# Kernel tuning notes

Hardware: AMD Instinct MI355X
Metric: run time of the kernel (lower is better)

Reference implementation:

```python
import jax, jax.numpy as jnp
import numpy as np

B, T, E, H, G = 8, 1024, 1024, 16, 4
D = E // H
SCALING = D ** -0.5
READER_W = 0.1  # reader_group_weight


def _heads(x):
    # [B, T, E] -> [B, H, T, D]
    return x.reshape(B, T, H, D).transpose(0, 2, 1, 3)


def setup_inputs() -> dict:
    key = jax.random.key(0)
    ks = jax.random.split(key, 16)
    s = 0.02
    return {
        "hidden_states": jax.random.normal(ks[0], (B, T, E), jnp.float32),
        "reader_token": jax.random.randint(ks[1], (B,), 0, G, dtype=jnp.int32),
        # shared (generic) projections, torch Linear convention: y = x @ W.T + b
        "Wq": jax.random.normal(ks[2], (E, E), jnp.float32) * s,
        "bq": jnp.zeros((E,), jnp.float32),
        "Wk": jax.random.normal(ks[3], (E, E), jnp.float32) * s,
        "bk": jnp.zeros((E,), jnp.float32),
        "Wv": jax.random.normal(ks[4], (E, E), jnp.float32) * s,
        "bv": jnp.zeros((E,), jnp.float32),
        "Wo": jax.random.normal(ks[5], (E, E), jnp.float32) * s,
        "bo": jnp.zeros((E,), jnp.float32),
        # stacked per-reader-group expert projections [G, E, E]
        "RWq": jax.random.normal(ks[6], (G, E, E), jnp.float32) * s,
        "Rbq": jnp.zeros((G, E), jnp.float32),
        "RWk": jax.random.normal(ks[7], (G, E, E), jnp.float32) * s,
        "Rbk": jnp.zeros((G, E), jnp.float32),
        "RWv": jax.random.normal(ks[8], (G, E, E), jnp.float32) * s,
        "Rbv": jnp.zeros((G, E), jnp.float32),
    }


def reference(hidden_states, reader_token, Wq, bq, Wk, bk, Wv, bv, Wo, bo,
              RWq, Rbq, RWk, Rbk, RWv, Rbv):
    hs = hidden_states
    # --- generic attention probs (shared weights) ---
    q = _heads((hs @ Wq.T + bq) * SCALING)          # [B,H,T,D]
    k = _heads(hs @ Wk.T + bk)                       # [B,H,T,D]
    v = _heads(hs @ Wv.T + bv)                       # [B,H,T,D]
    gen_probs = jax.nn.softmax(jnp.einsum('bhtd,bhsd->bhts', q, k), axis=-1)
    # --- reader-group attention probs (per-sample routed weights) ---
    Wq_b = RWq[reader_token]                          # [B,E,E]
    Wk_b = RWk[reader_token]
    q_r = _heads((jnp.einsum('bte,boe->bto', hs, Wq_b) + Rbq[reader_token][:, None, :]) * SCALING)
    k_r = _heads(jnp.einsum('bte,boe->bto', hs, Wk_b) + Rbk[reader_token][:, None, :])
    rdr_probs = jax.nn.softmax(jnp.einsum('bhtd,bhsd->bhts', q_r, k_r), axis=-1)
    # --- weighted combine, then attend over GENERIC value states ---
    probs = (READER_W * rdr_probs + (1.0 - READER_W) * gen_probs) / 2.0
    attn = jnp.einsum('bhts,bhsd->bhtd', probs, v)    # [B,H,T,D]
    attn = attn.transpose(0, 2, 1, 3).reshape(B, T, E)
    return attn @ Wo.T + bo
```

## Files before the change

kernel.cpp:

```cpp
#include <hip/hip_runtime.h>
#include <stdint.h>

#define AS1 __attribute__((address_space(1)))
#define AS3 __attribute__((address_space(3)))

typedef __attribute__((ext_vector_type(8))) short bf16x8;
typedef __attribute__((ext_vector_type(4))) float f32x4;

#define NB 8
#define NT 1024
#define NE 1024
#define NH 16
#define BT (NB * NT)

__device__ __forceinline__ unsigned short f2bf(float f) {
    unsigned int u = __builtin_bit_cast(unsigned int, f);
    u += 0x7FFFu + ((u >> 16) & 1u);
    return (unsigned short)(u >> 16);
}
__device__ __forceinline__ unsigned int cvt_pk_bf16(float lo, float hi) {
    unsigned int r;
    asm("v_cvt_pk_bf16_f32 %0, %1, %2" : "=v"(r) : "v"(lo), "v"(hi));
    return r;
}

__global__ void k_cvt7(const float* __restrict__ hs, unsigned short* __restrict__ hsB,
                       const float* __restrict__ w1, unsigned short* __restrict__ w1B,
                       const float* __restrict__ w2, unsigned short* __restrict__ w2B,
                       const float* __restrict__ w3, unsigned short* __restrict__ w3B,
                       const float* __restrict__ w4, unsigned short* __restrict__ w4B,
                       const float* __restrict__ r1, unsigned short* __restrict__ r1B,
                       const float* __restrict__ r2, unsigned short* __restrict__ r2B)
{
    int blk = blockIdx.x;
    const float* s; unsigned short* d; int base;
    if      (blk < 8192)  { s = hs; d = hsB; base = 0; }
    else if (blk < 9216)  { s = w1; d = w1B; base = 8192; }
    else if (blk < 10240) { s = w2; d = w2B; base = 9216; }
    else if (blk < 11264) { s = w3; d = w3B; base = 10240; }
    else if (blk < 12288) { s = w4; d = w4B; base = 11264; }
    else if (blk < 16384) { s = r1; d = r1B; base = 12288; }
    else                  { s = r2; d = r2B; base = 16384; }
    int i = ((blk - base) * 256 + threadIdx.x) * 4;
    float4 f = *reinterpret_cast<const float4*>(s + i);
    ushort4 o;
    o.x = f2bf(f.x); o.y = f2bf(f.y); o.z = f2bf(f.z); o.w = f2bf(f.w);
    *reinterpret_cast<ushort4*>(d + i) = o;
}

struct GJob {
    const unsigned short* W;
    const float* bias;
    void* out;
    float scale;
    int routed;
};

template <bool OUT_F32>
__global__ __launch_bounds__(512, 2)
void k_gemm256(const unsigned short* __restrict__ A,
               GJob j0, GJob j1, GJob j2, GJob j3, GJob j4,
               const int* __restrict__ rt)
{
    __shared__ __attribute__((aligned(16))) unsigned short LB[2][2][2][128 * 64];

    const int flat = blockIdx.x;
    const int xcd = flat & 7;
    const int l   = flat >> 3;
    const int pz  = l >> 4;
    const int r   = l & 15;
    const int by  = xcd * 4 + (r >> 2);
    const int bx  = r & 3;
    const int m0 = by << 8, n0 = bx << 8;

    GJob jb = j0;
    if (pz == 1) jb = j1;
    else if (pz == 2) jb = j2;
    else if (pz == 3) jb = j3;
    else if (pz == 4) jb = j4;
    int g = jb.routed ? rt[m0 >> 10] : 0;
    const unsigned short* Wg = jb.W + (size_t)g * NE * NE;

    const int tid  = threadIdx.x;
    const int wid  = tid >> 6;
    const int lane = tid & 63;
    const int frow = lane & 15;
    const int g4   = lane >> 4;
    const int wm = wid >> 2, wn = wid & 3;

    const int rh0  = tid >> 3;
    const int swz8 = ((tid & 7) ^ (rh0 & 7)) * 8;
    const unsigned short* baseA = A  + (size_t)m0 * NE;
    const unsigned short* baseB = Wg + (size_t)n0 * NE;

    auto STAGE = [&](int d, int mat, int half, int kt) {
        const unsigned short* base = mat ? baseB : baseA;
#pragma unroll
        for (int j = 0; j < 2; ++j) {
            const unsigned short* src =
                base + (size_t)(half * 128 + rh0 + j * 64) * NE + kt * 64 + swz8;
            __builtin_amdgcn_global_load_lds((AS1 void*)src,
                (AS3 void*)&LB[d][mat][half][(wid * 64 + j * 512) * 8], 16, 0, 0);
        }
    };

    f32x4 acc[8][4];
#pragma unroll
    for (int m = 0; m < 8; ++m)
#pragma unroll
        for (int n = 0; n < 4; ++n) acc[m][n] = (f32x4){0.f, 0.f, 0.f, 0.f};

    bf16x8 a4[4], b4[4];
    auto RDA = [&](int d, int mh, int kh) {
#pragma unroll
        for (int mf = 0; mf < 4; ++mf) {
            int rh = mh * 64 + mf * 16 + frow;
            int off = rh * 64 + (((kh * 4 + g4) ^ (frow & 7)) * 8);
            a4[mf] = *reinterpret_cast<const bf16x8*>(&LB[d][0][wm][off]);
        }
    };
    auto RDB = [&](int d, int kh) {
#pragma unroll
        for (int nf = 0; nf < 4; ++nf) {
            int rh = (wn & 1) * 64 + nf * 16 + frow;
            int off = rh * 64 + (((kh * 4 + g4) ^ (frow & 7)) * 8);
            b4[nf] = *reinterpret_cast<const bf16x8*>(&LB[d][1][wn >> 1][off]);
        }
    };
    auto MM = [&](int mh) {
        __builtin_amdgcn_s_setprio(1);
#pragma unroll
        for (int mf = 0; mf < 4; ++mf)
#pragma unroll
            for (int nf = 0; nf < 4; ++nf)
                acc[mh * 4 + mf][nf] =
                    __builtin_amdgcn_mfma_f32_16x16x32_bf16(a4[mf], b4[nf], acc[mh * 4 + mf][nf], 0, 0, 0);
        __builtin_amdgcn_s_setprio(0);
    };

#define BARX __builtin_amdgcn_s_barrier()
#define LGK0 asm volatile("s_waitcnt lgkmcnt(0)" ::: "memory")
#define VMC2 asm volatile("s_waitcnt vmcnt(2)" ::: "memory")
#define VMC0 asm volatile("s_waitcnt vmcnt(0)" ::: "memory")

    STAGE(0, 0, 0, 0); STAGE(0, 0, 1, 0); STAGE(0, 1, 0, 0); STAGE(0, 1, 1, 0);
    STAGE(1, 1, 0, 1);
    VMC2; BARX;

#pragma unroll 1
    for (int i = 0; i < 8; ++i) {
        const int t = 2 * i;
        const bool pre = (i < 7);
        RDA(0, 0, 0); RDB(0, 0); STAGE(1, 1, 1, t + 1); STAGE(1, 0, 1, t + 1);
        BARX; LGK0; MM(0); BARX;
        RDA(0, 1, 0); STAGE(1, 0, 0, t + 1);
        BARX; LGK0; MM(1); BARX;
        RDA(0, 0, 1); RDB(0, 1);
        BARX; LGK0; MM(0); BARX;
        RDA(0, 1, 1); if (pre) STAGE(0, 1, 0, t + 2);
        BARX; LGK0; MM(1); if (pre) { VMC2; } else { VMC0; } BARX;
        RDA(1, 0, 0); RDB(1, 0); if (pre) { STAGE(0, 1, 1, t + 2); STAGE(0, 0, 1, t + 2); }
        BARX; LGK0; MM(0); BARX;
        RDA(1, 1, 0); if (pre) STAGE(0, 0, 0, t + 2);
        BARX; LGK0; MM(1); BARX;
        RDA(1, 0, 1); RDB(1, 1);
        BARX; LGK0; MM(0); BARX;
        RDA(1, 1, 1); if (pre) STAGE(1, 1, 0, t + 3);
        BARX; LGK0; MM(1); VMC2; BARX;
    }
#undef BARX
#undef LGK0
#undef VMC2
#undef VMC0

    const float* biasg = jb.bias + (size_t)(jb.routed ? (rt[m0 >> 10]) : 0) * NE;
#pragma unroll
    for (int am = 0; am < 8; ++am) {
        int row = m0 + wm * 128 + am * 16 + g4 * 4;
#pragma unroll
        for (int nf = 0; nf < 4; ++nf) {
            int col = n0 + wn * 64 + nf * 16 + frow;
            float bv = biasg[col];
            f32x4 v = acc[am][nf];
#pragma unroll
            for (int r2 = 0; r2 < 4; ++r2) {
                float val = (v[r2] + bv) * jb.scale;
                if (OUT_F32)
                    ((float*)jb.out)[(size_t)(row + r2) * NE + col] = val;
                else
                    ((unsigned short*)jb.out)[(size_t)(row + r2) * NE + col] = f2bf(val);
            }
        }
    }
}

__global__ void k_vtrans(const unsigned short* __restrict__ V, unsigned short* __restrict__ Vt) {
    __shared__ unsigned short tile[64][65];
    const int blk = blockIdx.x;
    const int bh = blk >> 4;
    const int b = bh >> 4;
    const int h = bh & 15;
    const int s0 = (blk & 15) * 64;
    const int tid = threadIdx.x;
#pragma unroll
    for (int i = 0; i < 2; ++i) {
        int seg = tid + i * 256;
        int row = seg >> 3;
        int c8 = (seg & 7) * 8;
        const unsigned short* src = V + (size_t)(b * NT + s0 + row) * NE + h * 64 + c8;
        ushort4 u0 = *reinterpret_cast<const ushort4*>(src);
        ushort4 u1 = *reinterpret_cast<const ushort4*>(src + 4);
        tile[row][c8 + 0] = u0.x; tile[row][c8 + 1] = u0.y;
        tile[row][c8 + 2] = u0.z; tile[row][c8 + 3] = u0.w;
        tile[row][c8 + 4] = u1.x; tile[row][c8 + 5] = u1.y;
        tile[row][c8 + 6] = u1.z; tile[row][c8 + 7] = u1.w;
    }
    __syncthreads();
#pragma unroll
    for (int i = 0; i < 2; ++i) {
        int seg = tid + i * 256;
        int drow = seg >> 3;
        int s8 = (seg & 7) * 8;
        ushort4 u0, u1;
        u0.x = tile[s8 + 0][drow]; u0.y = tile[s8 + 1][drow];
        u0.z = tile[s8 + 2][drow]; u0.w = tile[s8 + 3][drow];
        u1.x = tile[s8 + 4][drow]; u1.y = tile[s8 + 5][drow];
        u1.z = tile[s8 + 6][drow]; u1.w = tile[s8 + 7][drow];
        unsigned short* dst = Vt + (size_t)(bh * 64 + drow) * NT + s0 + s8;
        *reinterpret_cast<ushort4*>(dst) = u0;
        *reinterpret_cast<ushort4*>(dst + 4) = u1;
    }
}

__global__ __launch_bounds__(512, 4)
void k_attn(const unsigned short* __restrict__ Q,
            const unsigned short* __restrict__ K,
            const unsigned short* __restrict__ Qr,
            const unsigned short* __restrict__ Kr,
            const unsigned short* __restrict__ Vt,
            unsigned short* __restrict__ attnO)
{
    constexpr int PLD = 40;
    __shared__ __attribute__((aligned(16))) unsigned short KV[2][3 * 4096];
    __shared__ __attribute__((aligned(16))) unsigned short Pga[8][16 * PLD];
    __shared__ __attribute__((aligned(16))) unsigned short Pra[8][16 * PLD];

    const int blk = (blockIdx.x & 7) * 128 + (blockIdx.x >> 3);
    const int tile = blk & 7;
    const int bh = blk >> 3;
    const int b = bh >> 4;
    const int h = bh & 15;
    const int wid = threadIdx.x >> 6;
    const int lane = threadIdx.x & 63;
    const int frow = lane & 15;
    const int g4 = lane >> 4;
    const int f7 = frow & 7;
    const int fk8 = g4 * 8;
    const int t0 = tile * 128 + wid * 16;

    const size_t qoff = (size_t)(b * NT + t0 + frow) * NE + h * 64;
    const bf16x8 qf0 = *reinterpret_cast<const bf16x8*>(Q + qoff + fk8);
    const bf16x8 qf1 = *reinterpret_cast<const bf16x8*>(Q + qoff + 32 + fk8);
    const bf16x8 qr0 = *reinterpret_cast<const bf16x8*>(Qr + qoff + fk8);
    const bf16x8 qr1 = *reinterpret_cast<const bf16x8*>(Qr + qoff + 32 + fk8);

    const unsigned short* Kb  = K  + (size_t)b * NT * NE + h * 64;
    const unsigned short* Krb = Kr + (size_t)b * NT * NE + h * 64;
    const unsigned short* Vtb = Vt + (size_t)bh * 64 * NT;
    unsigned short* PgRow = &Pga[wid][0] + frow * PLD;
    unsigned short* PrRow = &Pra[wid][0] + frow * PLD;

    f32x4 og[4], orr[4];
    float lgp = 0.f, lrp = 0.f;
#pragma unroll
    for (int i = 0; i < 4; ++i) {
        og[i] = (f32x4){0.f, 0.f, 0.f, 0.f};
        orr[i] = (f32x4){0.f, 0.f, 0.f, 0.f};
    }

    const int srow = threadIdx.x >> 3;
    const int scb8 = ((threadIdx.x & 7) ^ (srow & 7)) * 8;
    auto stage = [&](int buf, int s0) {
        const unsigned short* sK = Kb  + (size_t)(s0 + srow) * NE + scb8;
        const unsigned short* sR = Krb + (size_t)(s0 + srow) * NE + scb8;
        const unsigned short* sV = Vtb + (size_t)srow * NT + s0 + scb8;
        __builtin_amdgcn_global_load_lds((AS1 void*)sK, (AS3 void*)(&KV[buf][wid * 512]), 16, 0, 0);
        __builtin_amdgcn_global_load_lds((AS1 void*)sR, (AS3 void*)(&KV[buf][4096 + wid * 512]), 16, 0, 0);
        __builtin_amdgcn_global_load_lds((AS1 void*)sV, (AS3 void*)(&KV[buf][8192 + wid * 512]), 16, 0, 0);
    };

    stage(0, 0);
    __syncthreads();
    int cur = 0;
    const f32x4 z = (f32x4){0.f, 0.f, 0.f, 0.f};
#pragma unroll 1
    for (int t = 0; t < NT / 64; ++t) {
        if (t < NT / 64 - 1) stage(cur ^ 1, (t + 1) * 64);
        const unsigned short* Kl  = &KV[cur][0];
        const unsigned short* Krl = &KV[cur][4096];
        const unsigned short* Vl  = &KV[cur][8192];

        f32x4 sg[4], sr[4];
#pragma unroll
        for (int nf = 0; nf < 4; ++nf) {
            const int ro = (nf * 16 + frow) * 64;
            bf16x8 kA = *reinterpret_cast<const bf16x8*>(Kl + ro + ((g4 ^ f7) * 8));
            bf16x8 kB = *reinterpret_cast<const bf16x8*>(Kl + ro + (((4 + g4) ^ f7) * 8));
            bf16x8 rA = *reinterpret_cast<const bf16x8*>(Krl + ro + ((g4 ^ f7) * 8));
            bf16x8 rB = *reinterpret_cast<const bf16x8*>(Krl + ro + (((4 + g4) ^ f7) * 8));
            sg[nf] = __builtin_amdgcn_mfma_f32_16x16x32_bf16(kA, qf0, z, 0, 0, 0);
            sg[nf] = __builtin_amdgcn_mfma_f32_16x16x32_bf16(kB, qf1, sg[nf], 0, 0, 0);
            sr[nf] = __builtin_amdgcn_mfma_f32_16x16x32_bf16(rA, qr0, z, 0, 0, 0);
            sr[nf] = __builtin_amdgcn_mfma_f32_16x16x32_bf16(rB, qr1, sr[nf], 0, 0, 0);
        }

#pragma unroll
        for (int hh = 0; hh < 2; ++hh) {
#pragma unroll
            for (int j = 0; j < 2; ++j) {
                const int nf = 2 * hh + j;
                float g0 = __expf(sg[nf][0]), g1 = __expf(sg[nf][1]);
                float g2 = __expf(sg[nf][2]), g3 = __expf(sg[nf][3]);
                lgp += (g0 + g1) + (g2 + g3);
                uint2 wg;
                wg.x = cvt_pk_bf16(g0, g1);
                wg.y = cvt_pk_bf16(g2, g3);
                *reinterpret_cast<uint2*>(PgRow + j * 16 + g4 * 4) = wg;
                float r0 = __expf(sr[nf][0]), r1 = __expf(sr[nf][1]);
                float r2 = __expf(sr[nf][2]), r3 = __expf(sr[nf][3]);
                lrp += (r0 + r1) + (r2 + r3);
                uint2 wr;
                wr.x = cvt_pk_bf16(r0, r1);
                wr.y = cvt_pk_bf16(r2, r3);
                *reinterpret_cast<uint2*>(PrRow + j * 16 + g4 * 4) = wr;
            }
            asm volatile("s_waitcnt lgkmcnt(0)" ::: "memory");
            bf16x8 pg = *reinterpret_cast<const bf16x8*>(PgRow + fk8);
            bf16x8 pr = *reinterpret_cast<const bf16x8*>(PrRow + fk8);
            __builtin_amdgcn_s_setprio(1);
#pragma unroll
            for (int nf2 = 0; nf2 < 4; ++nf2) {
                const int vo = (nf2 * 16 + frow) * 64;
                bf16x8 v = *reinterpret_cast<const bf16x8*>(Vl + vo + (((4 * hh + g4) ^ f7) * 8));
                og[nf2]  = __builtin_amdgcn_mfma_f32_16x16x32_bf16(pg, v, og[nf2], 0, 0, 0);
                orr[nf2] = __builtin_amdgcn_mfma_f32_16x16x32_bf16(pr, v, orr[nf2], 0, 0, 0);
            }
            __builtin_amdgcn_s_setprio(0);
        }

        __syncthreads();
        cur ^= 1;
    }

    lgp += __shfl_xor(lgp, 16); lgp += __shfl_xor(lgp, 32);
    lrp += __shfl_xor(lrp, 16); lrp += __shfl_xor(lrp, 32);
    float ig = 0.45f / lgp, ir = 0.05f / lrp;
    float igr[4], irr[4];
#pragma unroll
    for (int r = 0; r < 4; ++r) {
        igr[r] = __shfl(ig, g4 * 4 + r);
        irr[r] = __shfl(ir, g4 * 4 + r);
    }
#pragma unroll
    for (int nf2 = 0; nf2 < 4; ++nf2) {
#pragma unroll
        for (int r = 0; r < 4; ++r) {
            float val = og[nf2][r] * igr[r] + orr[nf2][r] * irr[r];
            int tq = t0 + g4 * 4 + r;
            attnO[(size_t)(b * NT + tq) * NE + h * 64 + nf2 * 16 + frow] = f2bf(val);
        }
    }
}

extern "C" void kernel_launch(void* const* d_in, const int* in_sizes, int n_in,
                              void* d_out, int out_size, void* d_ws, size_t ws_size,
                              hipStream_t stream)
{
    const float* hs  = (const float*)d_in[0];
    const int*   rt  = (const int*)d_in[1];
    const float* Wq  = (const float*)d_in[2];
    const float* bq  = (const float*)d_in[3];
    const float* Wk  = (const float*)d_in[4];
    const float* bk  = (const float*)d_in[5];
    const float* Wv  = (const float*)d_in[6];
    const float* bv  = (const float*)d_in[7];
    const float* Wo  = (const float*)d_in[8];
    const float* bo  = (const float*)d_in[9];
    const float* RWq = (const float*)d_in[10];
    const float* Rbq = (const float*)d_in[11];
    const float* RWk = (const float*)d_in[12];
    const float* Rbk = (const float*)d_in[13];

    unsigned short* w = (unsigned short*)d_ws;
    const size_t NBT = (size_t)BT * NE;
    const size_t NW  = (size_t)NE * NE;
    unsigned short* hsB  = w; w += NBT;
    unsigned short* Qb   = w; w += NBT;
    unsigned short* Kb   = w; w += NBT;
    unsigned short* Vb   = w; w += NBT;
    unsigned short* Qrb  = w; w += NBT;
    unsigned short* Krb  = w; w += NBT;
    unsigned short* Vtb  = w; w += NBT;
    unsigned short* atb  = w; w += NBT;
    unsigned short* WqB  = w; w += NW;
    unsigned short* WkB  = w; w += NW;
    unsigned short* WvB  = w; w += NW;
    unsigned short* WoB  = w; w += NW;
    unsigned short* RWqB = w; w += 4 * NW;
    unsigned short* RWkB = w; w += 4 * NW;

    k_cvt7<<<dim3(20480), dim3(256), 0, stream>>>(hs, hsB, Wq, WqB, Wk, WkB, Wv, WvB,
                                                  Wo, WoB, RWq, RWqB, RWk, RWkB);

    GJob jq  = { WqB,  bq,  Qb,  0.125f, 0 };
    GJob jk  = { WkB,  bk,  Kb,  1.0f,   0 };
    GJob jv  = { WvB,  bv,  Vb,  1.0f,   0 };
    GJob jrq = { RWqB, Rbq, Qrb, 0.125f, 1 };
    GJob jrk = { RWkB, Rbk, Krb, 1.0f,   1 };
    k_gemm256<false><<<dim3(640), dim3(512), 0, stream>>>(hsB, jq, jk, jv, jrq, jrk, rt);

    k_vtrans<<<dim3(NB * NH * 16), dim3(256), 0, stream>>>(Vb, Vtb);
    k_attn<<<dim3(NB * NH * 8), dim3(512), 0, stream>>>(Qb, Kb, Qrb, Krb, Vtb, atb);

    GJob jo = { WoB, bo, d_out, 1.0f, 0 };
    k_gemm256<true><<<dim3(128), dim3(512), 0, stream>>>(atb, jo, jo, jo, jo, jo, nullptr);
}
```

Baseline: 241.1 us.

## Rework projection GEMM into 256x128 tiles with triple-buffered K=32 pipeline

Replaces the 256x256-tile, 8-wave GEMM with a 256x128-tile, 4-wave kernel. It uses a three-stage LDS ring of K=32 slices with a new XOR swizzle, and prefetches two slices ahead under vmcnt(6) waits. Grid sizes double, which gives more blocks for better CU fill, especially on the 128-block output projection. In exchange, each block reuses less data from a smaller tile and the K loop has more barriers per unit of work.

After: 243.9 us. No clear change (+1.2%).

```diff
diff --git a/kernel.cpp b/kernel.cpp
--- a/kernel.cpp
+++ b/kernel.cpp
@@ -57,21 +57,22 @@
 };
 
 template <bool OUT_F32>
-__global__ __launch_bounds__(512, 2)
-void k_gemm256(const unsigned short* __restrict__ A,
-               GJob j0, GJob j1, GJob j2, GJob j3, GJob j4,
-               const int* __restrict__ rt)
+__global__ __launch_bounds__(256, 2)
+void k_gemmP(const unsigned short* __restrict__ A,
+             GJob j0, GJob j1, GJob j2, GJob j3, GJob j4,
+             const int* __restrict__ rt)
 {
-    __shared__ __attribute__((aligned(16))) unsigned short LB[2][2][2][128 * 64];
+    __shared__ __attribute__((aligned(16))) unsigned short LA[3][256 * 32];
+    __shared__ __attribute__((aligned(16))) unsigned short LBb[3][128 * 32];
 
     const int flat = blockIdx.x;
     const int xcd = flat & 7;
     const int l   = flat >> 3;
-    const int pz  = l >> 4;
-    const int r   = l & 15;
-    const int by  = xcd * 4 + (r >> 2);
-    const int bx  = r & 3;
-    const int m0 = by << 8, n0 = bx << 8;
+    const int pz  = l >> 5;
+    const int r   = l & 31;
+    const int by  = xcd * 4 + (r >> 3);
+    const int bx  = r & 7;
+    const int m0 = by << 8, n0 = bx << 7;
 
     GJob jb = j0;
     if (pz == 1) jb = j1;
@@ -86,21 +87,31 @@
     const int lane = tid & 63;
     const int frow = lane & 15;
     const int g4   = lane >> 4;
-    const int wm = wid >> 2, wn = wid & 3;
-
-    const int rh0  = tid >> 3;
-    const int swz8 = ((tid & 7) ^ (rh0 & 7)) * 8;
+    const int wm = wid >> 1, wn = wid & 1;
+
     const unsigned short* baseA = A  + (size_t)m0 * NE;
     const unsigned short* baseB = Wg + (size_t)n0 * NE;
 
-    auto STAGE = [&](int d, int mat, int half, int kt) {
-        const unsigned short* base = mat ? baseB : baseA;
+    auto STAGE_A = [&](int buf, int kt) {
+#pragma unroll
+        for (int j = 0; j < 4; ++j) {
+            int c = tid + j * 256;
+            int row = c >> 2, cb = c & 3;
+            const unsigned short* src = baseA + (size_t)row * NE + kt * 32
+                                        + ((cb ^ ((row >> 1) & 3)) * 8);
+            __builtin_amdgcn_global_load_lds((AS1 void*)src,
+                (AS3 void*)(&LA[buf][0] + c * 8), 16, 0, 0);
+        }
+    };
+    auto STAGE_B = [&](int buf, int kt) {
 #pragma unroll
         for (int j = 0; j < 2; ++j) {
-            const unsigned short* src =
-                base + (size_t)(half * 128 + rh0 + j * 64) * NE + kt * 64 + swz8;
+            int c = tid + j * 256;
+            int row = c >> 2, cb = c & 3;
+            const unsigned short* src = baseB + (size_t)row * NE + kt * 32
+                                        + ((cb ^ ((row >> 1) & 3)) * 8);
             __builtin_amdgcn_global_load_lds((AS1 void*)src,
-                (AS3 void*)&LB[d][mat][half][(wid * 64 + j * 512) * 8], 16, 0, 0);
+                (AS3 void*)(&LBb[buf][0] + c * 8), 16, 0, 0);
         }
     };
 
@@ -111,20 +122,20 @@
         for (int n = 0; n < 4; ++n) acc[m][n] = (f32x4){0.f, 0.f, 0.f, 0.f};
 
     bf16x8 a4[4], b4[4];
-    auto RDA = [&](int d, int mh, int kh) {
+    auto RDA = [&](int buf, int mh) {
 #pragma unroll
         for (int mf = 0; mf < 4; ++mf) {
-            int rh = mh * 64 + mf * 16 + frow;
-            int off = rh * 64 + (((kh * 4 + g4) ^ (frow & 7)) * 8);
-            a4[mf] = *reinterpret_cast<const bf16x8*>(&LB[d][0][wm][off]);
-        }
-    };
-    auto RDB = [&](int d, int kh) {
+            int row = wm * 128 + mh * 64 + mf * 16 + frow;
+            a4[mf] = *reinterpret_cast<const bf16x8*>(
+                &LA[buf][row * 32 + ((g4 ^ ((row >> 1) & 3)) * 8)]);
+        }
+    };
+    auto RDB = [&](int buf) {
 #pragma unroll
         for (int nf = 0; nf < 4; ++nf) {
-            int rh = (wn & 1) * 64 + nf * 16 + frow;
-            int off = rh * 64 + (((kh * 4 + g4) ^ (frow & 7)) * 8);
-            b4[nf] = *reinterpret_cast<const bf16x8*>(&LB[d][1][wn >> 1][off]);
+            int row = wn * 64 + nf * 16 + frow;
+            b4[nf] = *reinterpret_cast<const bf16x8*>(
+                &LBb[buf][row * 32 + ((g4 ^ ((row >> 1) & 3)) * 8)]);
         }
     };
     auto MM = [&](int mh) {
@@ -140,40 +151,33 @@
 
 #define BARX __builtin_amdgcn_s_barrier()
 #define LGK0 asm volatile("s_waitcnt lgkmcnt(0)" ::: "memory")
-#define VMC2 asm volatile("s_waitcnt vmcnt(2)" ::: "memory")
+#define VMC6 asm volatile("s_waitcnt vmcnt(6)" ::: "memory")
 #define VMC0 asm volatile("s_waitcnt vmcnt(0)" ::: "memory")
 
-    STAGE(0, 0, 0, 0); STAGE(0, 0, 1, 0); STAGE(0, 1, 0, 0); STAGE(0, 1, 1, 0);
-    STAGE(1, 1, 0, 1);
-    VMC2; BARX;
-
+    STAGE_A(0, 0); STAGE_B(0, 0); STAGE_A(1, 1); STAGE_B(1, 1);
+    VMC6; BARX;
+
+    int bt = 0;
 #pragma unroll 1
-    for (int i = 0; i < 8; ++i) {
-        const int t = 2 * i;
-        const bool pre = (i < 7);
-        RDA(0, 0, 0); RDB(0, 0); STAGE(1, 1, 1, t + 1); STAGE(1, 0, 1, t + 1);
+    for (int t = 0; t < 32; ++t) {
+        const int b2 = (bt + 2 >= 3) ? bt - 1 : bt + 2;
+        const bool pre = (t + 2 < 32);
+        RDA(bt, 0); RDB(bt);
+        if (pre) STAGE_A(b2, t + 2);
         BARX; LGK0; MM(0); BARX;
-        RDA(0, 1, 0); STAGE(1, 0, 0, t + 1);
-        BARX; LGK0; MM(1); BARX;
-        RDA(0, 0, 1); RDB(0, 1);
-        BARX; LGK0; MM(0); BARX;
-        RDA(0, 1, 1); if (pre) STAGE(0, 1, 0, t + 2);
-        BARX; LGK0; MM(1); if (pre) { VMC2; } else { VMC0; } BARX;
-        RDA(1, 0, 0); RDB(1, 0); if (pre) { STAGE(0, 1, 1, t + 2); STAGE(0, 0, 1, t + 2); }
-        BARX; LGK0; MM(0); BARX;
-        RDA(1, 1, 0); if (pre) STAGE(0, 0, 0, t + 2);
-        BARX; LGK0; MM(1); BARX;
-        RDA(1, 0, 1); RDB(1, 1);
-        BARX; LGK0; MM(0); BARX;
-        RDA(1, 1, 1); if (pre) STAGE(1, 1, 0, t + 3);
-        BARX; LGK0; MM(1); VMC2; BARX;
+        RDA(bt, 1);
+        if (pre) STAGE_B(b2, t + 2);
+        BARX; LGK0; MM(1);
+        if (t < 30) { VMC6; } else if (t == 30) { VMC0; }
+        BARX;
+        bt = (bt + 1 >= 3) ? 0 : bt + 1;
     }
 #undef BARX
 #undef LGK0
-#undef VMC2
+#undef VMC6
 #undef VMC0
 
-    const float* biasg = jb.bias + (size_t)(jb.routed ? (rt[m0 >> 10]) : 0) * NE;
+    const float* biasg = jb.bias + (size_t)g * NE;
 #pragma unroll
     for (int am = 0; am < 8; ++am) {
         int row = m0 + wm * 128 + am * 16 + g4 * 4;
@@ -417,11 +421,11 @@
     GJob jv  = { WvB,  bv,  Vb,  1.0f,   0 };
     GJob jrq = { RWqB, Rbq, Qrb, 0.125f, 1 };
     GJob jrk = { RWkB, Rbk, Krb, 1.0f,   1 };
-    k_gemm256<false><<<dim3(640), dim3(512), 0, stream>>>(hsB, jq, jk, jv, jrq, jrk, rt);
+    k_gemmP<false><<<dim3(1280), dim3(256), 0, stream>>>(hsB, jq, jk, jv, jrq, jrk, rt);
 
     k_vtrans<<<dim3(NB * NH * 16), dim3(256), 0, stream>>>(Vb, Vtb);
     k_attn<<<dim3(NB * NH * 8), dim3(512), 0, stream>>>(Qb, Kb, Qrb, Krb, Vtb, atb);
 
     GJob jo = { WoB, bo, d_out, 1.0f, 0 };
-    k_gemm256<true><<<dim3(128), dim3(512), 0, stream>>>(atb, jo, jo, jo, jo, jo, nullptr);
-}
+    k_gemmP<true><<<dim3(256), dim3(256), 0, stream>>>(atb, jo, jo, jo, jo, jo, nullptr);
+}
```
